# Optimization experiments

Hardware: AMD Instinct MI355X
Metric: run time of the kernel (lower is better)

The kernel has to match this reference:

```python
import jax, jax.numpy as jnp
import numpy as np

N_NODES = 100000
N_EDGES = 1600000
D_IN = 128
D_HID = 128


def gcn_conv(x, src, dst, W, b, n_nodes):
    """PyG-style GCNConv: out = D^{-1/2} (A + I) D^{-1/2} (x @ W) + b.

    src/dst already include self-loops.
    """
    deg = jax.ops.segment_sum(jnp.ones_like(src, dtype=x.dtype), dst,
                              num_segments=n_nodes)
    dinv = jnp.where(deg > 0, deg ** -0.5, 0.0)
    norm = dinv[src] * dinv[dst]              # [E]
    h = x @ W                                  # [N, d_out]
    msg = h[src] * norm[:, None]               # gather + scale, [E, d_out]
    out = jax.ops.segment_sum(msg, dst, num_segments=n_nodes)
    return out + b


def setup_inputs() -> dict:
    key = jax.random.key(0)
    k1, k2, k3, k4 = jax.random.split(key, 4)
    x = jax.random.normal(k1, (N_NODES, D_IN), dtype=jnp.float32)
    edge_index = jax.random.randint(k2, (2, N_EDGES), 0, N_NODES, dtype=jnp.int64)
    s1 = (1.0 / np.sqrt(D_IN)).astype(np.float32)
    s2 = (1.0 / np.sqrt(D_HID)).astype(np.float32)
    W1 = jax.random.normal(k3, (D_IN, D_HID), dtype=jnp.float32) * s1
    b1 = jnp.zeros((D_HID,), dtype=jnp.float32)
    W2 = jax.random.normal(k4, (D_HID, D_HID), dtype=jnp.float32) * s2
    b2 = jnp.zeros((D_HID,), dtype=jnp.float32)
    return {"x": x, "edge_index": edge_index, "W1": W1, "b1": b1,
            "W2": W2, "b2": b2}


def reference(x, edge_index, W1, b1, W2, b2):
    n_nodes = x.shape[0]
    loops = jnp.arange(n_nodes, dtype=edge_index.dtype)
    src = jnp.concatenate([edge_index[0], loops])  # self-loops, as PyG default
    dst = jnp.concatenate([edge_index[1], loops])
    h = gcn_conv(x, src, dst, W1, b1, n_nodes)
    h = gcn_conv(h, src, dst, W2, b2, n_nodes)
    return h
```

## Files before the change

kernel.cpp:

```cpp
#include <hip/hip_runtime.h>

#define N_NODES 100000
#define N_EDGES 1600000

#define NBIN 196
#define BINCAP 9216
#define NPB 4096
#define EPT 16
#define BPT 36
#define PBLK ((N_EDGES + NPB - 1) / NPB)
#define GG ((N_NODES + 63) / 64)

typedef unsigned int uint;
typedef unsigned short u16;
typedef unsigned long long u64;
typedef __attribute__((ext_vector_type(8))) short bf16x8;
typedef __attribute__((ext_vector_type(4))) float f32x4;

__device__ __forceinline__ uint bf16_rtne(float f) {
  uint u = __float_as_uint(f);
  return (u + 0x7fffu + ((u >> 16) & 1u)) >> 16;
}


__global__ __launch_bounds__(256) void k_prepw(const float* __restrict__ W1, const float* __restrict__ W2,
                                               uint* __restrict__ S1, uint* __restrict__ S2,
                                               int* __restrict__ bin_cur) {
  if (blockIdx.x == 0 && blockIdx.y == 0 && threadIdx.x < NBIN) bin_cur[threadIdx.x] = 0;
  int u = blockIdx.x * 256 + threadIdx.x;
  const float* W = blockIdx.y ? W2 : W1;
  uint* S = blockIdx.y ? S2 : S1;
  int lane = u & 63;
  int kcnt = u >> 6;
  int kc = kcnt & 3;
  int nt = kcnt >> 2;
  int n = nt * 16 + (lane & 15);
  int k0 = kc * 32 + (lane >> 4) * 8;
  float f[8];
#pragma unroll
  for (int j = 0; j < 8; ++j) f[j] = W[(size_t)(k0 + j) * 128 + n];
  uint4 pk;
  pk.x = bf16_rtne(f[0]) | (bf16_rtne(f[1]) << 16);
  pk.y = bf16_rtne(f[2]) | (bf16_rtne(f[3]) << 16);
  pk.z = bf16_rtne(f[4]) | (bf16_rtne(f[5]) << 16);
  pk.w = bf16_rtne(f[6]) | (bf16_rtne(f[7]) << 16);
  ((uint4*)S)[u] = pk;
}


__device__ __forceinline__ void part_body(int bid, const int* __restrict__ ei,
                                          int* __restrict__ bin_cur, uint* __restrict__ stage,
                                          uint* smem) {
  uint* hist  = smem;
  uint* wbase = smem + 4 * NBIN;
  uint* lcur  = smem + 8 * NBIN;
  const int t = threadIdx.x;
  const int w = t >> 6;
  const int e0 = bid * NPB;
  for (int i = t; i < 4 * NBIN; i += 256) { hist[i] = 0; lcur[i] = 0; }
  __syncthreads();
  uint d[EPT];
#pragma unroll
  for (int j = 0; j < EPT; ++j) {
    int e = e0 + j * 256 + t;
    d[j] = (e < N_EDGES) ? (uint)ei[N_EDGES + e] : 0xFFFFFFFFu;
    if (d[j] != 0xFFFFFFFFu) atomicAdd(&hist[w * NBIN + (d[j] >> 9)], 1u);
  }
  __syncthreads();
  if (t < NBIN) {
    uint h0 = hist[t], h1 = hist[NBIN + t], h2 = hist[2 * NBIN + t], h3 = hist[3 * NBIN + t];
    uint tot = h0 + h1 + h2 + h3;
    uint g = tot ? (uint)atomicAdd(&bin_cur[t], (int)tot) : 0u;
    wbase[t] = g;
    wbase[NBIN + t] = g + h0;
    wbase[2 * NBIN + t] = g + h0 + h1;
    wbase[3 * NBIN + t] = g + h0 + h1 + h2;
  }
  __syncthreads();
#pragma unroll
  for (int j = 0; j < EPT; ++j) {
    if (d[j] != 0xFFFFFFFFu) {
      int e = e0 + j * 256 + t;
      uint s = (uint)ei[e];
      uint b = d[j] >> 9;
      uint pos = wbase[w * NBIN + b] + atomicAdd(&lcur[w * NBIN + b], 1u);
      if (pos < BINCAP)
        stage[(size_t)b * BINCAP + pos] = s | ((d[j] & 511u) << 17);
    }
  }
}

__device__ __forceinline__ void gemm_body(int gb, const float* __restrict__ x,
                                          const uint* __restrict__ Wsw, u16* __restrict__ OutH,
                                          uint* smem) {
  uint* As = smem;
  uint* Bs = smem + 4096;
  const int tid = threadIdx.x;
  const int R = gb * 64;
  {
    const uint4* src = (const uint4*)Wsw;
    uint4* dst = (uint4*)Bs;
#pragma unroll
    for (int v = 0; v < 8; ++v) dst[tid + v * 256] = src[tid + v * 256];
  }
  const int unit = tid & 15;
  const int kc_s = unit >> 2;
  const int quad_s = unit & 3;
#pragma unroll
  for (int pass = 0; pass < 4; ++pass) {
    int row = pass * 16 + (tid >> 4);
    int gr = R + row;
    if (gr >= N_NODES) gr = N_NODES - 1;
    const float* srcr = x + (size_t)gr * 128 + unit * 8;
    float4 f0 = ((const float4*)srcr)[0];
    float4 f1 = ((const float4*)srcr)[1];
    uint4 pk;
    pk.x = bf16_rtne(f0.x) | (bf16_rtne(f0.y) << 16);
    pk.y = bf16_rtne(f0.z) | (bf16_rtne(f0.w) << 16);
    pk.z = bf16_rtne(f1.x) | (bf16_rtne(f1.y) << 16);
    pk.w = bf16_rtne(f1.z) | (bf16_rtne(f1.w) << 16);
    int lane_t = quad_s * 16 + (row & 15);
    *(uint4*)&As[((pass * 4 + kc_s) * 64 + lane_t) * 4] = pk;
  }
  __syncthreads();

  const int w = tid >> 6;
  const int lane = tid & 63;
  bf16x8 a0 = *(bf16x8*)&As[((w * 4 + 0) * 64 + lane) * 4];
  bf16x8 a1 = *(bf16x8*)&As[((w * 4 + 1) * 64 + lane) * 4];
  bf16x8 a2 = *(bf16x8*)&As[((w * 4 + 2) * 64 + lane) * 4];
  bf16x8 a3 = *(bf16x8*)&As[((w * 4 + 3) * 64 + lane) * 4];
  f32x4 acc[8];
#pragma unroll
  for (int nt = 0; nt < 8; ++nt) acc[nt] = (f32x4){0.f, 0.f, 0.f, 0.f};
#pragma unroll
  for (int nt = 0; nt < 8; ++nt) {
    bf16x8 b0 = *(bf16x8*)&Bs[((nt * 4 + 0) * 64 + lane) * 4];
    bf16x8 b1 = *(bf16x8*)&Bs[((nt * 4 + 1) * 64 + lane) * 4];
    bf16x8 b2 = *(bf16x8*)&Bs[((nt * 4 + 2) * 64 + lane) * 4];
    bf16x8 b3 = *(bf16x8*)&Bs[((nt * 4 + 3) * 64 + lane) * 4];
    acc[nt] = __builtin_amdgcn_mfma_f32_16x16x32_bf16(a0, b0, acc[nt], 0, 0, 0);
    acc[nt] = __builtin_amdgcn_mfma_f32_16x16x32_bf16(a1, b1, acc[nt], 0, 0, 0);
    acc[nt] = __builtin_amdgcn_mfma_f32_16x16x32_bf16(a2, b2, acc[nt], 0, 0, 0);
    acc[nt] = __builtin_amdgcn_mfma_f32_16x16x32_bf16(a3, b3, acc[nt], 0, 0, 0);
  }
  const int colb = lane & 15;
  const int quad = lane >> 4;
#pragma unroll
  for (int nt = 0; nt < 8; ++nt) {
#pragma unroll
    for (int r = 0; r < 4; ++r) {
      int gr = R + w * 16 + quad * 4 + r;
      if (gr < N_NODES)
        OutH[(size_t)gr * 128 + nt * 16 + colb] = (u16)bf16_rtne(acc[nt][r]);
    }
  }
}

__global__ __launch_bounds__(256) void k_pg(const int* __restrict__ ei, int* __restrict__ bin_cur,
                                            uint* __restrict__ stage,
                                            const float* __restrict__ x, const uint* __restrict__ Wsw,
                                            u16* __restrict__ OutH) {
  __shared__ uint smem[12288];
  if ((int)blockIdx.x < PBLK) part_body(blockIdx.x, ei, bin_cur, stage, smem);
  else                        gemm_body(blockIdx.x - PBLK, x, Wsw, OutH, smem);
}


__global__ __launch_bounds__(256) void k_bin2(const int* __restrict__ bin_cur, const uint* __restrict__ stage,
                                              float* __restrict__ dinv, int* __restrict__ rowptr,
                                              int* __restrict__ ep) {
  __shared__ int cnt[512];
  __shared__ int sd[256];
  __shared__ int curs[512];
  const int b = blockIdx.x, t = threadIdx.x;
  int vg = (t < NBIN) ? min(bin_cur[t], BINCAP) : 0;
  sd[t] = vg;
  __syncthreads();
  for (int off = 1; off < 256; off <<= 1) {
    int a = (t >= off) ? sd[t - off] : 0;
    __syncthreads();
    sd[t] += a;
    __syncthreads();
  }
  const int eb = (b > 0) ? sd[b - 1] : 0;
  if (b == 0 && t == 0) rowptr[N_NODES] = sd[NBIN - 1];
  __syncthreads();

  cnt[t] = 0; cnt[t + 256] = 0;
  __syncthreads();
  const int n = min(bin_cur[b], BINCAP);
  const uint* sb = stage + (size_t)b * BINCAP;
  uint r[BPT];
#pragma unroll
  for (int j = 0; j < BPT; ++j) {
    int i = j * 256 + t;
    r[j] = (i < n) ? sb[i] : 0xFFFFFFFFu;
  }
#pragma unroll
  for (int j = 0; j < BPT; ++j)
    if (r[j] != 0xFFFFFFFFu) atomicAdd(&cnt[r[j] >> 17], 1);
  __syncthreads();
  int v0 = cnt[t * 2], v1 = cnt[t * 2 + 1];
  int s = v0 + v1;
  sd[t] = s;
  __syncthreads();
  for (int off = 1; off < 256; off <<= 1) {
    int a = (t >= off) ? sd[t - off] : 0;
    __syncthreads();
    sd[t] += a;
    __syncthreads();
  }
  int run = sd[t] - s;
  int c0 = eb + run, c1 = eb + run + v0;
  int g0 = b * 512 + t * 2;
  if (g0 < N_NODES) {
    rowptr[g0] = c0;
    dinv[g0] = rsqrtf((float)(v0 + 1));
  }
  if (g0 + 1 < N_NODES) {
    rowptr[g0 + 1] = c1;
    dinv[g0 + 1] = rsqrtf((float)(v1 + 1));
  }
  curs[t * 2] = c0; curs[t * 2 + 1] = c1;
  __syncthreads();
#pragma unroll
  for (int j = 0; j < BPT; ++j)
    if (r[j] != 0xFFFFFFFFu) {
      int pos = atomicAdd(&curs[r[j] >> 17], 1);
      ep[pos] = (int)(r[j] & 0x1FFFFu);
    }
}


__device__ __forceinline__ void bacc(float& ax, float& ay, uint v, float w) {
  ax += w * __uint_as_float(v << 16);
  ay += w * __uint_as_float(v & 0xffff0000u);
}

__device__ __forceinline__ void agg_node(const uint* __restrict__ hb, const float* __restrict__ dinv,
                                         const int* __restrict__ ep, int node, int lane,
                                         int beg, int end, float dn, float& ax, float& ay) {
  uint selfv = hb[(size_t)node * 64 + lane];
  bacc(ax, ay, selfv, dn);
  int e = beg;
  for (; e + 8 <= end; e += 8) {
    int p[8];
#pragma unroll
    for (int j = 0; j < 8; ++j) p[j] = ep[e + j];
    float wt[8];
#pragma unroll
    for (int j = 0; j < 8; ++j) wt[j] = dinv[p[j]];
    uint v[8];
#pragma unroll
    for (int j = 0; j < 8; ++j) v[j] = hb[(size_t)p[j] * 64 + lane];
#pragma unroll
    for (int j = 0; j < 8; ++j) bacc(ax, ay, v[j], wt[j]);
  }
  if (e + 4 <= end) {
    int p[4];
#pragma unroll
    for (int j = 0; j < 4; ++j) p[j] = ep[e + j];
    float wt[4];
#pragma unroll
    for (int j = 0; j < 4; ++j) wt[j] = dinv[p[j]];
    uint v[4];
#pragma unroll
    for (int j = 0; j < 4; ++j) v[j] = hb[(size_t)p[j] * 64 + lane];
#pragma unroll
    for (int j = 0; j < 4; ++j) bacc(ax, ay, v[j], wt[j]);
    e += 4;
  }
  for (; e < end; ++e) {
    int p = ep[e];
    float wt = dinv[p];
    uint v = hb[(size_t)p * 64 + lane];
    bacc(ax, ay, v, wt);
  }
}


__global__ __launch_bounds__(1024) void k_aggm(const uint* __restrict__ hb, const float* __restrict__ dinv,
                                               const int* __restrict__ rowptr, const int* __restrict__ ep,
                                               const float* __restrict__ bias, const uint* __restrict__ Wsw,
                                               u16* __restrict__ outH) {
  __shared__ uint Abf[16 * 64];
  const int w = threadIdx.x >> 6;
  const int lane = threadIdx.x & 63;
  const int nb = blockIdx.x * 16;
  {
    const int node = nb + w;
    const int beg = rowptr[node];
    const int end = rowptr[node + 1];
    const float dn = dinv[node];
    float ax = 0.f, ay = 0.f;
    agg_node(hb, dinv, ep, node, lane, beg, end, dn, ax, ay);
    int c = lane * 2;
    float rx = dn * ax + bias[c];
    float ry = dn * ay + bias[c + 1];
    uint pk = bf16_rtne(rx) | (bf16_rtne(ry) << 16);
    Abf[(w * 64 + lane) ^ ((w & 7) << 2)] = pk;
  }
  __syncthreads();
  if (w >= 8) return;
  const int row = lane & 15;
  const int kq = lane >> 4;
  bf16x8 a[4];
#pragma unroll
  for (int kc = 0; kc < 4; ++kc) {
    int ui = row * 64 + kc * 16 + kq * 4;
    a[kc] = *(bf16x8*)&Abf[ui ^ ((row & 7) << 2)];
  }
  f32x4 acc = (f32x4){0.f, 0.f, 0.f, 0.f};
#pragma unroll
  for (int kc = 0; kc < 4; ++kc) {
    bf16x8 bfr = *(const bf16x8*)((const uint4*)Wsw + (w * 4 + kc) * 64 + lane);
    acc = __builtin_amdgcn_mfma_f32_16x16x32_bf16(a[kc], bfr, acc, 0, 0, 0);
  }
  const int colb = lane & 15;
  const int quad = lane >> 4;
#pragma unroll
  for (int r2 = 0; r2 < 4; ++r2) {
    int gr = nb + quad * 4 + r2;
    outH[(size_t)gr * 128 + w * 16 + colb] = (u16)bf16_rtne(acc[r2]);
  }
}


__global__ __launch_bounds__(256) void k_agg(const uint* __restrict__ hb, const float* __restrict__ dinv,
                                             const int* __restrict__ rowptr, const int* __restrict__ ep,
                                             const float* __restrict__ bias,
                                             float* __restrict__ outf) {
  int wid = threadIdx.x >> 6;
  int lane = threadIdx.x & 63;
  int node = blockIdx.x * 4 + wid;
  if (node >= N_NODES) return;
  int beg = rowptr[node];
  int end = rowptr[node + 1];
  float dn = dinv[node];
  float ax = 0.f, ay = 0.f;
  agg_node(hb, dinv, ep, node, lane, beg, end, dn, ax, ay);
  int c = lane * 2;
  float2 o;
  o.x = dn * ax + bias[c];
  o.y = dn * ay + bias[c + 1];
  *(float2*)(outf + (size_t)node * 128 + c) = o;
}


extern "C" void kernel_launch(void* const* d_in, const int* in_sizes, int n_in,
                              void* d_out, int out_size, void* d_ws, size_t ws_size,
                              hipStream_t stream) {
  const float* x  = (const float*)d_in[0];
  const int*   ei = (const int*)d_in[1];
  const float* W1 = (const float*)d_in[2];
  const float* b1 = (const float*)d_in[3];
  const float* W2 = (const float*)d_in[4];
  const float* b2 = (const float*)d_in[5];
  float* out = (float*)d_out;

  char* p = (char*)d_ws;
  uint*  hb     = (uint*)p;  p += (size_t)N_NODES * 64 * sizeof(uint);
  int*   ep     = (int*)p;   p += (size_t)N_EDGES * sizeof(int);
  uint*  wsw1   = (uint*)p;  p += 8192 * sizeof(uint);
  uint*  wsw2   = (uint*)p;  p += 8192 * sizeof(uint);
  float* dinv   = (float*)p; p += (size_t)N_NODES * sizeof(float);
  int*   rowptr = (int*)p;   p += (size_t)(N_NODES + 1) * sizeof(int);
  int*   bin_cur= (int*)p;   p += (size_t)NBIN * sizeof(int);
  p = (char*)(((uintptr_t)p + 255) & ~(uintptr_t)255);
  uint*  stage  = (uint*)p;
  uint*  hb2    = (uint*)p;

  k_prepw<<<dim3(8, 2), 256, 0, stream>>>(W1, W2, wsw1, wsw2, bin_cur);
  k_pg<<<PBLK + GG, 256, 0, stream>>>(ei, bin_cur, stage, x, wsw1, (u16*)hb);
  k_bin2<<<NBIN, 256, 0, stream>>>(bin_cur, stage, dinv, rowptr, ep);
  k_aggm<<<N_NODES / 16, 1024, 0, stream>>>(hb, dinv, rowptr, ep, b1, wsw2, (u16*)hb2);
  k_agg<<<(N_NODES + 3) / 4, 256, 0, stream>>>(hb2, dinv, rowptr, ep, b2, out);
}
```

Before: 299.4 us.

## Fold W1·W2 into one weight product and drop the intermediate MFMA layer

Because there is no nonlinearity between the two GCN layers, the change precomputes W1@W2 (and b1@W2) in the prep kernel. It applies a single fused projection to x before aggregation, so the second layer becomes pure aggregation. The per-node weighted bias term is rebuilt from a stored scalar (sum of normalized weights) in the final aggregation. This removes the matmul stage inside the middle aggregation kernel and its 1024-thread blocks, at the cost of a serial 128-length dot product per thread in the prep kernel and different rounding (bf16 of the fused product).

```diff
diff --git a/kernel.cpp b/kernel.cpp
--- a/kernel.cpp
+++ b/kernel.cpp
@@ -23,13 +23,11 @@
 }
 
 
-__global__ __launch_bounds__(256) void k_prepw(const float* __restrict__ W1, const float* __restrict__ W2,
-                                               uint* __restrict__ S1, uint* __restrict__ S2,
-                                               int* __restrict__ bin_cur) {
-  if (blockIdx.x == 0 && blockIdx.y == 0 && threadIdx.x < NBIN) bin_cur[threadIdx.x] = 0;
+__global__ __launch_bounds__(256) void k_prep(const float* __restrict__ W1, const float* __restrict__ W2,
+                                              const float* __restrict__ b1,
+                                              uint* __restrict__ S12, float* __restrict__ bW2,
+                                              int* __restrict__ bin_cur) {
   int u = blockIdx.x * 256 + threadIdx.x;
-  const float* W = blockIdx.y ? W2 : W1;
-  uint* S = blockIdx.y ? S2 : S1;
   int lane = u & 63;
   int kcnt = u >> 6;
   int kc = kcnt & 3;
@@ -38,13 +36,27 @@
   int k0 = kc * 32 + (lane >> 4) * 8;
   float f[8];
 #pragma unroll
-  for (int j = 0; j < 8; ++j) f[j] = W[(size_t)(k0 + j) * 128 + n];
+  for (int j = 0; j < 8; ++j) f[j] = 0.f;
+  for (int m = 0; m < 128; ++m) {
+    float w2v = W2[(size_t)m * 128 + n];
+#pragma unroll
+    for (int j = 0; j < 8; ++j) f[j] += W1[(size_t)(k0 + j) * 128 + m] * w2v;
+  }
   uint4 pk;
   pk.x = bf16_rtne(f[0]) | (bf16_rtne(f[1]) << 16);
   pk.y = bf16_rtne(f[2]) | (bf16_rtne(f[3]) << 16);
   pk.z = bf16_rtne(f[4]) | (bf16_rtne(f[5]) << 16);
   pk.w = bf16_rtne(f[6]) | (bf16_rtne(f[7]) << 16);
-  ((uint4*)S)[u] = pk;
+  ((uint4*)S12)[u] = pk;
+  if (blockIdx.x == 0) {
+    if (threadIdx.x < NBIN) bin_cur[threadIdx.x] = 0;
+    if (threadIdx.x < 128) {
+      int c = threadIdx.x;
+      float acc = 0.f;
+      for (int m = 0; m < 128; ++m) acc += b1[m] * W2[(size_t)m * 128 + c];
+      bW2[c] = acc;
+    }
+  }
 }
 
 
@@ -240,7 +252,7 @@
 
 __device__ __forceinline__ void agg_node(const uint* __restrict__ hb, const float* __restrict__ dinv,
                                          const int* __restrict__ ep, int node, int lane,
-                                         int beg, int end, float dn, float& ax, float& ay) {
+                                         int beg, int end, float dn, float& ax, float& ay, float& sw) {
   uint selfv = hb[(size_t)node * 64 + lane];
   bacc(ax, ay, selfv, dn);
   int e = beg;
@@ -255,7 +267,7 @@
 #pragma unroll
     for (int j = 0; j < 8; ++j) v[j] = hb[(size_t)p[j] * 64 + lane];
 #pragma unroll
-    for (int j = 0; j < 8; ++j) bacc(ax, ay, v[j], wt[j]);
+    for (int j = 0; j < 8; ++j) { bacc(ax, ay, v[j], wt[j]); sw += wt[j]; }
   }
   if (e + 4 <= end) {
     int p[4];
@@ -268,7 +280,7 @@
 #pragma unroll
     for (int j = 0; j < 4; ++j) v[j] = hb[(size_t)p[j] * 64 + lane];
 #pragma unroll
-    for (int j = 0; j < 4; ++j) bacc(ax, ay, v[j], wt[j]);
+    for (int j = 0; j < 4; ++j) { bacc(ax, ay, v[j], wt[j]); sw += wt[j]; }
     e += 4;
   }
   for (; e < end; ++e) {
@@ -276,61 +288,14 @@
     float wt = dinv[p];
     uint v = hb[(size_t)p * 64 + lane];
     bacc(ax, ay, v, wt);
-  }
-}
-
-
-__global__ __launch_bounds__(1024) void k_aggm(const uint* __restrict__ hb, const float* __restrict__ dinv,
-                                               const int* __restrict__ rowptr, const int* __restrict__ ep,
-                                               const float* __restrict__ bias, const uint* __restrict__ Wsw,
-                                               u16* __restrict__ outH) {
-  __shared__ uint Abf[16 * 64];
-  const int w = threadIdx.x >> 6;
-  const int lane = threadIdx.x & 63;
-  const int nb = blockIdx.x * 16;
-  {
-    const int node = nb + w;
-    const int beg = rowptr[node];
-    const int end = rowptr[node + 1];
-    const float dn = dinv[node];
-    float ax = 0.f, ay = 0.f;
-    agg_node(hb, dinv, ep, node, lane, beg, end, dn, ax, ay);
-    int c = lane * 2;
-    float rx = dn * ax + bias[c];
-    float ry = dn * ay + bias[c + 1];
-    uint pk = bf16_rtne(rx) | (bf16_rtne(ry) << 16);
-    Abf[(w * 64 + lane) ^ ((w & 7) << 2)] = pk;
-  }
-  __syncthreads();
-  if (w >= 8) return;
-  const int row = lane & 15;
-  const int kq = lane >> 4;
-  bf16x8 a[4];
-#pragma unroll
-  for (int kc = 0; kc < 4; ++kc) {
-    int ui = row * 64 + kc * 16 + kq * 4;
-    a[kc] = *(bf16x8*)&Abf[ui ^ ((row & 7) << 2)];
-  }
-  f32x4 acc = (f32x4){0.f, 0.f, 0.f, 0.f};
-#pragma unroll
-  for (int kc = 0; kc < 4; ++kc) {
-    bf16x8 bfr = *(const bf16x8*)((const uint4*)Wsw + (w * 4 + kc) * 64 + lane);
-    acc = __builtin_amdgcn_mfma_f32_16x16x32_bf16(a[kc], bfr, acc, 0, 0, 0);
-  }
-  const int colb = lane & 15;
-  const int quad = lane >> 4;
-#pragma unroll
-  for (int r2 = 0; r2 < 4; ++r2) {
-    int gr = nb + quad * 4 + r2;
-    outH[(size_t)gr * 128 + w * 16 + colb] = (u16)bf16_rtne(acc[r2]);
-  }
-}
-
-
-__global__ __launch_bounds__(256) void k_agg(const uint* __restrict__ hb, const float* __restrict__ dinv,
-                                             const int* __restrict__ rowptr, const int* __restrict__ ep,
-                                             const float* __restrict__ bias,
-                                             float* __restrict__ outf) {
+    sw += wt;
+  }
+}
+
+
+__global__ __launch_bounds__(256) void k_agg1(const uint* __restrict__ hb, const float* __restrict__ dinv,
+                                              const int* __restrict__ rowptr, const int* __restrict__ ep,
+                                              u16* __restrict__ outb, float* __restrict__ sArr) {
   int wid = threadIdx.x >> 6;
   int lane = threadIdx.x & 63;
   int node = blockIdx.x * 4 + wid;
@@ -338,12 +303,34 @@
   int beg = rowptr[node];
   int end = rowptr[node + 1];
   float dn = dinv[node];
-  float ax = 0.f, ay = 0.f;
-  agg_node(hb, dinv, ep, node, lane, beg, end, dn, ax, ay);
+  float ax = 0.f, ay = 0.f, sw = 0.f;
+  agg_node(hb, dinv, ep, node, lane, beg, end, dn, ax, ay, sw);
+  int c = lane * 2;
+  uint pk = bf16_rtne(dn * ax) | (bf16_rtne(dn * ay) << 16);
+  *(uint*)(outb + (size_t)node * 128 + c) = pk;
+  if (lane == 0) sArr[node] = dn * (dn + sw);
+}
+
+
+__global__ __launch_bounds__(256) void k_agg2(const uint* __restrict__ hb, const float* __restrict__ dinv,
+                                              const int* __restrict__ rowptr, const int* __restrict__ ep,
+                                              const float* __restrict__ sArr, const float* __restrict__ bW2,
+                                              const float* __restrict__ b2,
+                                              float* __restrict__ outf) {
+  int wid = threadIdx.x >> 6;
+  int lane = threadIdx.x & 63;
+  int node = blockIdx.x * 4 + wid;
+  if (node >= N_NODES) return;
+  int beg = rowptr[node];
+  int end = rowptr[node + 1];
+  float dn = dinv[node];
+  float ax = 0.f, ay = 0.f, sw = 0.f;
+  agg_node(hb, dinv, ep, node, lane, beg, end, dn, ax, ay, sw);
+  float si = sArr[node];
   int c = lane * 2;
   float2 o;
-  o.x = dn * ax + bias[c];
-  o.y = dn * ay + bias[c + 1];
+  o.x = dn * ax + si * bW2[c] + b2[c];
+  o.y = dn * ay + si * bW2[c + 1] + b2[c + 1];
   *(float2*)(outf + (size_t)node * 128 + c) = o;
 }
 
@@ -363,17 +350,18 @@
   uint*  hb     = (uint*)p;  p += (size_t)N_NODES * 64 * sizeof(uint);
   int*   ep     = (int*)p;   p += (size_t)N_EDGES * sizeof(int);
   uint*  wsw1   = (uint*)p;  p += 8192 * sizeof(uint);
-  uint*  wsw2   = (uint*)p;  p += 8192 * sizeof(uint);
+  float* bW2    = (float*)p; p += 128 * sizeof(float);
   float* dinv   = (float*)p; p += (size_t)N_NODES * sizeof(float);
   int*   rowptr = (int*)p;   p += (size_t)(N_NODES + 1) * sizeof(int);
+  float* sArr   = (float*)p; p += (size_t)N_NODES * sizeof(float);
   int*   bin_cur= (int*)p;   p += (size_t)NBIN * sizeof(int);
   p = (char*)(((uintptr_t)p + 255) & ~(uintptr_t)255);
   uint*  stage  = (uint*)p;
-  uint*  hb2    = (uint*)p;
-
-  k_prepw<<<dim3(8, 2), 256, 0, stream>>>(W1, W2, wsw1, wsw2, bin_cur);
+  u16*   h1b    = (u16*)p;
+
+  k_prep<<<8, 256, 0, stream>>>(W1, W2, b1, wsw1, bW2, bin_cur);
   k_pg<<<PBLK + GG, 256, 0, stream>>>(ei, bin_cur, stage, x, wsw1, (u16*)hb);
   k_bin2<<<NBIN, 256, 0, stream>>>(bin_cur, stage, dinv, rowptr, ep);
-  k_aggm<<<N_NODES / 16, 1024, 0, stream>>>(hb, dinv, rowptr, ep, b1, wsw2, (u16*)hb2);
-  k_agg<<<(N_NODES + 3) / 4, 256, 0, stream>>>(hb2, dinv, rowptr, ep, b2, out);
-}
+  k_agg1<<<(N_NODES + 3) / 4, 256, 0, stream>>>(hb, dinv, rowptr, ep, h1b, sArr);
+  k_agg2<<<(N_NODES + 3) / 4, 256, 0, stream>>>((const uint*)h1b, dinv, rowptr, ep, sArr, bW2, b2, out);
+}
```

After: 294.5 us. About the same (-1.6%).
